# Performance work log

Measured on AMD Instinct MI355X. Metric: run time of the kernel, lower is better.

Reference implementation:

```python
import jax, jax.numpy as jnp
import numpy as np

B, N, P_EDGE = 2048, 64, 0.08


def setup_inputs() -> dict:
    key = jax.random.key(0)
    k1, _ = jax.random.split(key)
    u = jax.random.uniform(k1, (B, N, N))
    upper = jnp.triu(u < P_EDGE, k=1)
    A = (upper | jnp.swapaxes(upper, -1, -2)).astype(jnp.float32)  # symmetric, zero diag
    E = jnp.stack([1.0 - A, A], axis=-1)  # [B,N,N,2] one-hot edges
    node_mask = jnp.ones((B, N), dtype=jnp.float32)
    return {"E": E, "node_mask": node_mask}


def _diag(X):
    return jnp.diagonal(X, axis1=-2, axis2=-1)


def _trace(X):
    return _diag(X).sum(-1)


def reference(E, node_mask):
    A = E[..., 1:].sum(-1).astype(jnp.float32)  # [B,N,N]
    d = A.sum(-1)                               # degrees [B,N]
    k2 = A @ A
    k3 = k2 @ A
    k4 = k3 @ A
    k5 = k4 @ A
    k6 = k5 @ A

    c3 = _diag(k3)
    k3x = (c3 / 2)[..., None]
    k3y = (c3.sum(-1) / 6)[..., None]

    diag_a4 = _diag(k4)
    c4 = diag_a4 - d * (d - 1) - jnp.einsum('bij,bj->bi', A, d)
    k4x = (c4 / 2)[..., None]
    k4y = (c4.sum(-1) / 8)[..., None]

    diag_a5 = _diag(k5)
    tri = c3
    c5 = diag_a5 - 2 * tri * d - jnp.einsum('bij,bj->bi', A, tri) + tri
    k5x = (c5 / 2)[..., None]
    k5y = (c5.sum(-1) / 10)[..., None]

    t1 = _trace(k6)
    t2 = _trace(k3 ** 2)
    t3 = jnp.sum(A * k2 ** 2, axis=(-2, -1))
    d2 = _diag(k2)
    t4 = (d2 * diag_a4).sum(-1)
    t5 = _trace(k4)
    t6 = _trace(k3)
    t7 = (d2 ** 3).sum(-1)
    t8 = jnp.sum(k3, axis=(-2, -1))
    t9 = (d2 ** 2).sum(-1)
    t10 = _trace(k2)
    c6 = t1 - 3 * t2 + 9 * t3 - 6 * t4 + 6 * t5 - 4 * t6 + 4 * t7 + 3 * t8 - 12 * t9 + 4 * t10
    k6y = (c6 / 12)[..., None]

    x_cycles = jnp.concatenate([k3x, k4x, k5x], axis=-1)            # [B,N,3]
    y_cycles = jnp.concatenate([k3y, k4y, k5y, k6y], axis=-1)       # [B,4]

    x_cycles = x_cycles * node_mask[..., None] / 10.0
    y_cycles = y_cycles / 10.0
    x_cycles = jnp.minimum(x_cycles, 1.0)
    y_cycles = jnp.minimum(y_cycles, 1.0)
    return x_cycles, y_cycles
```

## Files before the change

### kernel.cpp

```cpp
#include <hip/hip_runtime.h>


typedef __attribute__((ext_vector_type(8))) short bf16x8;
typedef __attribute__((ext_vector_type(16))) float f32x16;

constexpr int BATCH = 2048;
constexpr int NN = 64;

__device__ __forceinline__ bf16x8 frag_ld(const unsigned short* buf, int row, int kb2) {
  const int idx = row * 64 + ((kb2 ^ (row & 7)) << 3);
  const uint4 v = *reinterpret_cast<const uint4*>(buf + idx);
  union { uint4 u; bf16x8 b; } cv; cv.u = v; return cv.b;
}

__global__ __launch_bounds__(64, 2) void node_cycle_kernel(
    const float4* __restrict__ E4,
    const float* __restrict__ nmask,
    float* __restrict__ out)
{
  const int b = blockIdx.x;
  const int lane = threadIdx.x;
  const int h = lane >> 5;
  const int c31 = lane & 31;

  __shared__ unsigned short bufA[64 * 64];
  __shared__ unsigned short bufK2[64 * 64];
  __shared__ float c3sh[NN];
  __shared__ uint2 rms[NN];

  const float4* __restrict__ Eb = E4 + (size_t)b * (NN * NN / 2);
  unsigned long long mA = 0ull, mB = 0ull;
  #pragma unroll
  for (int t = 0; t < 32; ++t) {
    const float4 f = Eb[t * 64 + lane];
    const int bit = 2 * t + h;
    mA |= (unsigned long long)(f.y > 0.5f) << bit;
    mB |= (unsigned long long)(f.w > 0.5f) << bit;
  }
  mA |= __shfl_xor(mA, 32);
  mB |= __shfl_xor(mB, 32);
  if (lane < 32) {
    rms[2 * lane]     = make_uint2((unsigned)mA, (unsigned)(mA >> 32));
    rms[2 * lane + 1] = make_uint2((unsigned)mB, (unsigned)(mB >> 32));
  }
  __syncthreads();
  const unsigned mlo = rms[lane].x, mhi = rms[lane].y;

  #pragma unroll
  for (int q = 0; q < 8; ++q) {
    unsigned w[4];
    #pragma unroll
    for (int p2 = 0; p2 < 4; ++p2) {
      const int c0 = q * 8 + p2 * 2;
      const unsigned b0 = (c0 < 32 ? (mlo >> c0) : (mhi >> (c0 - 32))) & 1u;
      const unsigned b1 = ((c0 + 1) < 32 ? (mlo >> (c0 + 1)) : (mhi >> (c0 + 1 - 32))) & 1u;
      w[p2] = (b0 ? 0x3F80u : 0u) | (b1 ? 0x3F800000u : 0u);
    }
    const int idx = lane * 64 + ((q ^ (lane & 7)) << 3);
    *reinterpret_cast<uint4*>(&bufA[idx]) = make_uint4(w[0], w[1], w[2], w[3]);
  }
  __syncthreads();

  bf16x8 Af[2][4];
  #pragma unroll
  for (int R = 0; R < 2; ++R)
    #pragma unroll
    for (int K = 0; K < 4; ++K)
      Af[R][K] = frag_ld(bufA, R * 32 + c31, 2 * K + h);

  f32x16 a00, a01, a10, a11;
  #pragma unroll
  for (int r = 0; r < 16; ++r) { a00[r] = 0.f; a01[r] = 0.f; a10[r] = 0.f; a11[r] = 0.f; }
  #pragma unroll
  for (int K = 0; K < 4; ++K) {
    a00 = __builtin_amdgcn_mfma_f32_32x32x16_bf16(Af[0][K], Af[0][K], a00, 0, 0, 0);
    a01 = __builtin_amdgcn_mfma_f32_32x32x16_bf16(Af[0][K], Af[1][K], a01, 0, 0, 0);
    a10 = __builtin_amdgcn_mfma_f32_32x32x16_bf16(Af[1][K], Af[0][K], a10, 0, 0, 0);
    a11 = __builtin_amdgcn_mfma_f32_32x32x16_bf16(Af[1][K], Af[1][K], a11, 0, 0, 0);
  }

  #define PACK_K2(ACC, R, C)                                                    \
  {                                                                             \
    const int c = (C) * 32 + c31;                                               \
    _Pragma("unroll")                                                           \
    for (int g = 0; g < 4; ++g) {                                               \
      const unsigned w0 = (__float_as_uint(ACC[4*g+1]) & 0xffff0000u) |         \
                          (__float_as_uint(ACC[4*g+0]) >> 16);                  \
      const unsigned w1 = (__float_as_uint(ACC[4*g+3]) & 0xffff0000u) |         \
                          (__float_as_uint(ACC[4*g+2]) >> 16);                  \
      const int bb = (4 * (R) + g) ^ (c & 7);                                   \
      *reinterpret_cast<uint2*>(&bufK2[c * 64 + bb * 8 + h * 4]) =              \
          make_uint2(w0, w1);                                                   \
    }                                                                           \
  }
  PACK_K2(a00, 0, 0) PACK_K2(a01, 0, 1) PACK_K2(a10, 1, 0) PACK_K2(a11, 1, 1)
  __syncthreads();

  bf16x8 Kf[2][4];
  #pragma unroll
  for (int R = 0; R < 2; ++R)
    #pragma unroll
    for (int K = 0; K < 4; ++K)
      Kf[R][K] = frag_ld(bufK2, R * 32 + c31, 2 * K + h);

  f32x16 d00, d01, d10, d11;
  #pragma unroll
  for (int r = 0; r < 16; ++r) { d00[r] = 0.f; d01[r] = 0.f; d10[r] = 0.f; d11[r] = 0.f; }
  #pragma unroll
  for (int K = 0; K < 4; ++K) {
    d00 = __builtin_amdgcn_mfma_f32_32x32x16_bf16(Kf[0][K], Af[0][K], d00, 0, 0, 0);
    d01 = __builtin_amdgcn_mfma_f32_32x32x16_bf16(Kf[0][K], Af[1][K], d01, 0, 0, 0);
    d10 = __builtin_amdgcn_mfma_f32_32x32x16_bf16(Kf[1][K], Af[0][K], d10, 0, 0, 0);
    d11 = __builtin_amdgcn_mfma_f32_32x32x16_bf16(Kf[1][K], Af[1][K], d11, 0, 0, 0);
  }

  float t1p = 0.f, t8p = 0.f;
  #define RED_T18(ACC)                                                          \
  { _Pragma("unroll") for (int r = 0; r < 16; ++r) {                            \
      const float v = ACC[r]; t1p = fmaf(v, v, t1p); t8p += v; } }
  RED_T18(d00) RED_T18(d01) RED_T18(d10) RED_T18(d11)

  const int dtarget = c31 - 4 * h;
  float c3d0 = 0.f, c3d1 = 0.f;
  #pragma unroll
  for (int r = 0; r < 16; ++r) {
    const int rowbase = (r & 3) + 8 * (r >> 2);
    c3d0 += (rowbase == dtarget) ? d00[r] : 0.f;
    c3d1 += (rowbase == dtarget) ? d11[r] : 0.f;
  }
  if (((c31 >> 2) & 1) == h) { c3sh[c31] = c3d0; c3sh[32 + c31] = c3d1; }

  #define PACK_K3(ACC, R, C)                                                    \
  {                                                                             \
    const int c = (C) * 32 + c31;                                               \
    _Pragma("unroll")                                                           \
    for (int g = 0; g < 4; ++g) {                                               \
      const unsigned u0 = ((unsigned)ACC[4*g+0]) | (((unsigned)ACC[4*g+1]) << 16); \
      const unsigned u1 = ((unsigned)ACC[4*g+2]) | (((unsigned)ACC[4*g+3]) << 16); \
      const int bb = (4 * (R) + g) ^ (c & 7);                                   \
      *reinterpret_cast<uint2*>(&bufA[c * 64 + bb * 8 + h * 4]) =               \
          make_uint2(u0, u1);                                                   \
    }                                                                           \
  }
  PACK_K3(d00, 0, 0) PACK_K3(d01, 0, 1) PACK_K3(d10, 1, 0) PACK_K3(d11, 1, 1)
  __syncthreads();

  float diag4 = 0.f, Ad = 0.f, diag5 = 0.f, t3p = 0.f, Atri = 0.f;
  #pragma unroll
  for (int bq = 0; bq < 8; ++bq) {
    const int idx = lane * 64 + ((bq ^ (lane & 7)) << 3);
    const uint4 vk2 = *reinterpret_cast<const uint4*>(&bufK2[idx]);
    const uint4 vk3 = *reinterpret_cast<const uint4*>(&bufA[idx]);
    const float4 c3a = *reinterpret_cast<const float4*>(&c3sh[bq * 8]);
    const float4 c3b = *reinterpret_cast<const float4*>(&c3sh[bq * 8 + 4]);
    const unsigned wk2[4] = {vk2.x, vk2.y, vk2.z, vk2.w};
    const unsigned wk3[4] = {vk3.x, vk3.y, vk3.z, vk3.w};
    const float c3v[8] = {c3a.x, c3a.y, c3a.z, c3a.w, c3b.x, c3b.y, c3b.z, c3b.w};
    #pragma unroll
    for (int e2 = 0; e2 < 4; ++e2) {
      const int j0 = bq * 8 + 2 * e2;
      const float k2lo = __uint_as_float(wk2[e2] << 16);
      const float k2hi = __uint_as_float(wk2[e2] & 0xffff0000u);
      const float k3lo = (float)(wk3[e2] & 0xffffu);
      const float k3hi = (float)(wk3[e2] >> 16);
      diag4 = fmaf(k2lo, k2lo, fmaf(k2hi, k2hi, diag4));
      Ad += k2lo + k2hi;
      diag5 = fmaf(k2lo, k3lo, fmaf(k2hi, k3hi, diag5));
      const unsigned b0 = (j0 < 32 ? (mlo >> j0) : (mhi >> (j0 - 32))) & 1u;
      const unsigned b1 = ((j0 + 1) < 32 ? (mlo >> (j0 + 1)) : (mhi >> (j0 + 1 - 32))) & 1u;
      const float s0 = b0 ? k2lo : 0.f;
      const float s1 = b1 ? k2hi : 0.f;
      t3p = fmaf(s0, k2lo, fmaf(s1, k2hi, t3p));
      Atri += (b0 ? c3v[2 * e2] : 0.f) + (b1 ? c3v[2 * e2 + 1] : 0.f);
    }
  }

  const float di  = (float)(__popc(mlo) + __popc(mhi));
  const float c3i = c3sh[lane];

  const float c4 = diag4 - di * (di - 1.f) - Ad;
  const float c5 = diag5 - 2.f * c3i * di - Atri + c3i;
  const float c6p = t1p + 3.f * t8p
            - 3.f * (c3i * c3i)
            + 9.f * t3p
            - 6.f * (di * diag4)
            + 6.f * diag4
            - 4.f * c3i
            + 4.f * (di * di * di)
            - 12.f * (di * di)
            + 4.f * di;

  float sc3 = c3i, sc4 = c4, sc5 = c5, sc6 = c6p;
  #pragma unroll
  for (int off = 32; off > 0; off >>= 1) {
    sc3 += __shfl_xor(sc3, off);
    sc4 += __shfl_xor(sc4, off);
    sc5 += __shfl_xor(sc5, off);
    sc6 += __shfl_xor(sc6, off);
  }

  const float m = nmask[b * NN + lane];
  float* xo = out + ((size_t)b * NN + lane) * 3;
  xo[0] = fminf(c3i * 0.5f * m * 0.1f, 1.f);
  xo[1] = fminf(c4 * 0.5f * m * 0.1f, 1.f);
  xo[2] = fminf(c5 * 0.5f * m * 0.1f, 1.f);

  if (lane == 0) {
    float4 y;
    y.x = fminf(sc3 * (1.f / 6.f)  * 0.1f, 1.f);
    y.y = fminf(sc4 * (1.f / 8.f)  * 0.1f, 1.f);
    y.z = fminf(sc5 * (1.f / 10.f) * 0.1f, 1.f);
    y.w = fminf(sc6 * (1.f / 12.f) * 0.1f, 1.f);
    *reinterpret_cast<float4*>(out + (size_t)BATCH * NN * 3 + b * 4) = y;
  }
}

extern "C" void kernel_launch(void* const* d_in, const int* in_sizes, int n_in,
                              void* d_out, int out_size, void* d_ws, size_t ws_size,
                              hipStream_t stream) {
  const float4* E4 = reinterpret_cast<const float4*>(d_in[0]);
  const float* nmask = reinterpret_cast<const float*>(d_in[1]);
  float* out = reinterpret_cast<float*>(d_out);
  node_cycle_kernel<<<BATCH, NN, 0, stream>>>(E4, nmask, out);
}
```

Baseline: 20.75 us.

## Split per-graph work across four wavefronts, one 32x32 MFMA tile each

Moves from one 64-thread wave per graph to four waves per block, each owning one 32x32 quadrant of the A^2 and A^3 products, with its own slice of the E load and bitmask build. The row reductions are split by column blocks across waves and combined through a shared accumulator array. The t1/t8 sums now come from the packed k3 values in the reduction pass rather than the MFMA accumulators. This raises memory-level parallelism and cuts per-wave serial MFMA chains, at the cost of extra block barriers and more LDS.

```diff
diff --git a/kernel.cpp b/kernel.cpp
--- a/kernel.cpp
+++ b/kernel.cpp
@@ -13,141 +13,139 @@
   union { uint4 u; bf16x8 b; } cv; cv.u = v; return cv.b;
 }
 
-__global__ __launch_bounds__(64, 2) void node_cycle_kernel(
+__global__ __launch_bounds__(256, 5) void node_cycle_kernel(
     const float4* __restrict__ E4,
     const float* __restrict__ nmask,
     float* __restrict__ out)
 {
   const int b = blockIdx.x;
-  const int lane = threadIdx.x;
+  const int tid = threadIdx.x;
+  const int lane = tid & 63;
+  const int w = tid >> 6;
   const int h = lane >> 5;
   const int c31 = lane & 31;
+  const int R = w >> 1, C = w & 1;
 
   __shared__ unsigned short bufA[64 * 64];
   __shared__ unsigned short bufK2[64 * 64];
+  __shared__ unsigned short sl[4][64];
+  __shared__ uint2 rms[NN];
   __shared__ float c3sh[NN];
-  __shared__ uint2 rms[NN];
+  __shared__ float accs[4][7][NN];
 
   const float4* __restrict__ Eb = E4 + (size_t)b * (NN * NN / 2);
-  unsigned long long mA = 0ull, mB = 0ull;
-  #pragma unroll
-  for (int t = 0; t < 32; ++t) {
-    const float4 f = Eb[t * 64 + lane];
-    const int bit = 2 * t + h;
-    mA |= (unsigned long long)(f.y > 0.5f) << bit;
-    mB |= (unsigned long long)(f.w > 0.5f) << bit;
-  }
-  mA |= __shfl_xor(mA, 32);
-  mB |= __shfl_xor(mB, 32);
+
+  unsigned mA = 0u, mB = 0u;
+  #pragma unroll
+  for (int q = 0; q < 8; ++q) {
+    const float4 f = Eb[w * 512 + q * 64 + lane];
+    const int bit = 2 * q + h;
+    mA |= (unsigned)(f.y > 0.5f) << bit;
+    mB |= (unsigned)(f.w > 0.5f) << bit;
+  }
+  mA |= (unsigned)__shfl_xor((int)mA, 32);
+  mB |= (unsigned)__shfl_xor((int)mB, 32);
   if (lane < 32) {
-    rms[2 * lane]     = make_uint2((unsigned)mA, (unsigned)(mA >> 32));
-    rms[2 * lane + 1] = make_uint2((unsigned)mB, (unsigned)(mB >> 32));
-  }
-  __syncthreads();
-  const unsigned mlo = rms[lane].x, mhi = rms[lane].y;
-
-  #pragma unroll
-  for (int q = 0; q < 8; ++q) {
-    unsigned w[4];
-    #pragma unroll
-    for (int p2 = 0; p2 < 4; ++p2) {
-      const int c0 = q * 8 + p2 * 2;
-      const unsigned b0 = (c0 < 32 ? (mlo >> c0) : (mhi >> (c0 - 32))) & 1u;
-      const unsigned b1 = ((c0 + 1) < 32 ? (mlo >> (c0 + 1)) : (mhi >> (c0 + 1 - 32))) & 1u;
-      w[p2] = (b0 ? 0x3F80u : 0u) | (b1 ? 0x3F800000u : 0u);
-    }
-    const int idx = lane * 64 + ((q ^ (lane & 7)) << 3);
-    *reinterpret_cast<uint4*>(&bufA[idx]) = make_uint4(w[0], w[1], w[2], w[3]);
-  }
-  __syncthreads();
-
-  bf16x8 Af[2][4];
-  #pragma unroll
-  for (int R = 0; R < 2; ++R)
-    #pragma unroll
-    for (int K = 0; K < 4; ++K)
-      Af[R][K] = frag_ld(bufA, R * 32 + c31, 2 * K + h);
-
-  f32x16 a00, a01, a10, a11;
-  #pragma unroll
-  for (int r = 0; r < 16; ++r) { a00[r] = 0.f; a01[r] = 0.f; a10[r] = 0.f; a11[r] = 0.f; }
+    sl[w][2 * lane]     = (unsigned short)mA;
+    sl[w][2 * lane + 1] = (unsigned short)mB;
+  }
+  __syncthreads();
+
+  if (tid < 128) {
+    const int c = tid >> 1, hf = tid & 1;
+    const unsigned v = (unsigned)sl[2 * hf][c] | ((unsigned)sl[2 * hf + 1][c] << 16);
+    if (hf == 0) rms[c].x = v; else rms[c].y = v;
+  }
+  __syncthreads();
+
+  const uint2 mr = rms[lane];
+
+  {
+    const unsigned word = (w < 2) ? mr.x : mr.y;
+    const unsigned bits16 = (word >> (16 * (w & 1))) & 0xffffu;
+    #pragma unroll
+    for (int e = 0; e < 2; ++e) {
+      const int bq = 2 * w + e;
+      unsigned wv[4];
+      #pragma unroll
+      for (int p2 = 0; p2 < 4; ++p2) {
+        const int c0 = e * 8 + p2 * 2;
+        const unsigned b0 = (bits16 >> c0) & 1u;
+        const unsigned b1 = (bits16 >> (c0 + 1)) & 1u;
+        wv[p2] = (b0 ? 0x3F80u : 0u) | (b1 ? 0x3F800000u : 0u);
+      }
+      const int idx = lane * 64 + ((bq ^ (lane & 7)) << 3);
+      *reinterpret_cast<uint4*>(&bufA[idx]) = make_uint4(wv[0], wv[1], wv[2], wv[3]);
+    }
+  }
+  __syncthreads();
+
+  bf16x8 Af[4], Bf[4];
   #pragma unroll
   for (int K = 0; K < 4; ++K) {
-    a00 = __builtin_amdgcn_mfma_f32_32x32x16_bf16(Af[0][K], Af[0][K], a00, 0, 0, 0);
-    a01 = __builtin_amdgcn_mfma_f32_32x32x16_bf16(Af[0][K], Af[1][K], a01, 0, 0, 0);
-    a10 = __builtin_amdgcn_mfma_f32_32x32x16_bf16(Af[1][K], Af[0][K], a10, 0, 0, 0);
-    a11 = __builtin_amdgcn_mfma_f32_32x32x16_bf16(Af[1][K], Af[1][K], a11, 0, 0, 0);
-  }
-
-  #define PACK_K2(ACC, R, C)                                                    \
-  {                                                                             \
-    const int c = (C) * 32 + c31;                                               \
-    _Pragma("unroll")                                                           \
-    for (int g = 0; g < 4; ++g) {                                               \
-      const unsigned w0 = (__float_as_uint(ACC[4*g+1]) & 0xffff0000u) |         \
-                          (__float_as_uint(ACC[4*g+0]) >> 16);                  \
-      const unsigned w1 = (__float_as_uint(ACC[4*g+3]) & 0xffff0000u) |         \
-                          (__float_as_uint(ACC[4*g+2]) >> 16);                  \
-      const int bb = (4 * (R) + g) ^ (c & 7);                                   \
-      *reinterpret_cast<uint2*>(&bufK2[c * 64 + bb * 8 + h * 4]) =              \
-          make_uint2(w0, w1);                                                   \
-    }                                                                           \
-  }
-  PACK_K2(a00, 0, 0) PACK_K2(a01, 0, 1) PACK_K2(a10, 1, 0) PACK_K2(a11, 1, 1)
-  __syncthreads();
-
-  bf16x8 Kf[2][4];
-  #pragma unroll
-  for (int R = 0; R < 2; ++R)
-    #pragma unroll
-    for (int K = 0; K < 4; ++K)
-      Kf[R][K] = frag_ld(bufK2, R * 32 + c31, 2 * K + h);
-
-  f32x16 d00, d01, d10, d11;
-  #pragma unroll
-  for (int r = 0; r < 16; ++r) { d00[r] = 0.f; d01[r] = 0.f; d10[r] = 0.f; d11[r] = 0.f; }
-  #pragma unroll
-  for (int K = 0; K < 4; ++K) {
-    d00 = __builtin_amdgcn_mfma_f32_32x32x16_bf16(Kf[0][K], Af[0][K], d00, 0, 0, 0);
-    d01 = __builtin_amdgcn_mfma_f32_32x32x16_bf16(Kf[0][K], Af[1][K], d01, 0, 0, 0);
-    d10 = __builtin_amdgcn_mfma_f32_32x32x16_bf16(Kf[1][K], Af[0][K], d10, 0, 0, 0);
-    d11 = __builtin_amdgcn_mfma_f32_32x32x16_bf16(Kf[1][K], Af[1][K], d11, 0, 0, 0);
-  }
-
+    Af[K] = frag_ld(bufA, R * 32 + c31, 2 * K + h);
+    Bf[K] = frag_ld(bufA, C * 32 + c31, 2 * K + h);
+  }
+  f32x16 acc;
+  #pragma unroll
+  for (int r = 0; r < 16; ++r) acc[r] = 0.f;
+  #pragma unroll
+  for (int K = 0; K < 4; ++K)
+    acc = __builtin_amdgcn_mfma_f32_32x32x16_bf16(Af[K], Bf[K], acc, 0, 0, 0);
+
+  {
+    const int c = C * 32 + c31;
+    #pragma unroll
+    for (int g = 0; g < 4; ++g) {
+      const unsigned w0 = (__float_as_uint(acc[4*g+1]) & 0xffff0000u) |
+                          (__float_as_uint(acc[4*g+0]) >> 16);
+      const unsigned w1 = (__float_as_uint(acc[4*g+3]) & 0xffff0000u) |
+                          (__float_as_uint(acc[4*g+2]) >> 16);
+      const int bb = (4 * R + g) ^ (c & 7);
+      *reinterpret_cast<uint2*>(&bufK2[c * 64 + bb * 8 + h * 4]) = make_uint2(w0, w1);
+    }
+  }
+  __syncthreads();
+
+  bf16x8 Kf[4];
+  #pragma unroll
+  for (int K = 0; K < 4; ++K)
+    Kf[K] = frag_ld(bufK2, R * 32 + c31, 2 * K + h);
+  f32x16 d;
+  #pragma unroll
+  for (int r = 0; r < 16; ++r) d[r] = 0.f;
+  #pragma unroll
+  for (int K = 0; K < 4; ++K)
+    d = __builtin_amdgcn_mfma_f32_32x32x16_bf16(Kf[K], Bf[K], d, 0, 0, 0);
+
+  if (R == C) {
+    const int dtarget = c31 - 4 * h;
+    float c3d = 0.f;
+    #pragma unroll
+    for (int r = 0; r < 16; ++r) {
+      const int rowbase = (r & 3) + 8 * (r >> 2);
+      c3d += (rowbase == dtarget) ? d[r] : 0.f;
+    }
+    if (((c31 >> 2) & 1) == h) c3sh[R * 32 + c31] = c3d;
+  }
+
+  {
+    const int c = C * 32 + c31;
+    #pragma unroll
+    for (int g = 0; g < 4; ++g) {
+      const unsigned u0 = ((unsigned)d[4*g+0]) | (((unsigned)d[4*g+1]) << 16);
+      const unsigned u1 = ((unsigned)d[4*g+2]) | (((unsigned)d[4*g+3]) << 16);
+      const int bb = (4 * R + g) ^ (c & 7);
+      *reinterpret_cast<uint2*>(&bufA[c * 64 + bb * 8 + h * 4]) = make_uint2(u0, u1);
+    }
+  }
+  __syncthreads();
+
+  float diag4 = 0.f, Ad = 0.f, diag5 = 0.f, t3p = 0.f, Atri = 0.f;
   float t1p = 0.f, t8p = 0.f;
-  #define RED_T18(ACC)                                                          \
-  { _Pragma("unroll") for (int r = 0; r < 16; ++r) {                            \
-      const float v = ACC[r]; t1p = fmaf(v, v, t1p); t8p += v; } }
-  RED_T18(d00) RED_T18(d01) RED_T18(d10) RED_T18(d11)
-
-  const int dtarget = c31 - 4 * h;
-  float c3d0 = 0.f, c3d1 = 0.f;
-  #pragma unroll
-  for (int r = 0; r < 16; ++r) {
-    const int rowbase = (r & 3) + 8 * (r >> 2);
-    c3d0 += (rowbase == dtarget) ? d00[r] : 0.f;
-    c3d1 += (rowbase == dtarget) ? d11[r] : 0.f;
-  }
-  if (((c31 >> 2) & 1) == h) { c3sh[c31] = c3d0; c3sh[32 + c31] = c3d1; }
-
-  #define PACK_K3(ACC, R, C)                                                    \
-  {                                                                             \
-    const int c = (C) * 32 + c31;                                               \
-    _Pragma("unroll")                                                           \
-    for (int g = 0; g < 4; ++g) {                                               \
-      const unsigned u0 = ((unsigned)ACC[4*g+0]) | (((unsigned)ACC[4*g+1]) << 16); \
-      const unsigned u1 = ((unsigned)ACC[4*g+2]) | (((unsigned)ACC[4*g+3]) << 16); \
-      const int bb = (4 * (R) + g) ^ (c & 7);                                   \
-      *reinterpret_cast<uint2*>(&bufA[c * 64 + bb * 8 + h * 4]) =               \
-          make_uint2(u0, u1);                                                   \
-    }                                                                           \
-  }
-  PACK_K3(d00, 0, 0) PACK_K3(d01, 0, 1) PACK_K3(d10, 1, 0) PACK_K3(d11, 1, 1)
-  __syncthreads();
-
-  float diag4 = 0.f, Ad = 0.f, diag5 = 0.f, t3p = 0.f, Atri = 0.f;
-  #pragma unroll
-  for (int bq = 0; bq < 8; ++bq) {
+  #pragma unroll
+  for (int e = 0; e < 2; ++e) {
+    const int bq = 2 * w + e;
     const int idx = lane * 64 + ((bq ^ (lane & 7)) << 3);
     const uint4 vk2 = *reinterpret_cast<const uint4*>(&bufK2[idx]);
     const uint4 vk3 = *reinterpret_cast<const uint4*>(&bufA[idx]);
@@ -166,52 +164,71 @@
       diag4 = fmaf(k2lo, k2lo, fmaf(k2hi, k2hi, diag4));
       Ad += k2lo + k2hi;
       diag5 = fmaf(k2lo, k3lo, fmaf(k2hi, k3hi, diag5));
-      const unsigned b0 = (j0 < 32 ? (mlo >> j0) : (mhi >> (j0 - 32))) & 1u;
-      const unsigned b1 = ((j0 + 1) < 32 ? (mlo >> (j0 + 1)) : (mhi >> (j0 + 1 - 32))) & 1u;
+      t1p = fmaf(k3lo, k3lo, fmaf(k3hi, k3hi, t1p));
+      t8p += k3lo + k3hi;
+      const unsigned b0 = (j0 < 32 ? (mr.x >> j0) : (mr.y >> (j0 - 32))) & 1u;
+      const unsigned b1 = ((j0 + 1) < 32 ? (mr.x >> (j0 + 1)) : (mr.y >> (j0 + 1 - 32))) & 1u;
       const float s0 = b0 ? k2lo : 0.f;
       const float s1 = b1 ? k2hi : 0.f;
       t3p = fmaf(s0, k2lo, fmaf(s1, k2hi, t3p));
       Atri += (b0 ? c3v[2 * e2] : 0.f) + (b1 ? c3v[2 * e2 + 1] : 0.f);
     }
   }
-
-  const float di  = (float)(__popc(mlo) + __popc(mhi));
-  const float c3i = c3sh[lane];
-
-  const float c4 = diag4 - di * (di - 1.f) - Ad;
-  const float c5 = diag5 - 2.f * c3i * di - Atri + c3i;
-  const float c6p = t1p + 3.f * t8p
-            - 3.f * (c3i * c3i)
-            + 9.f * t3p
-            - 6.f * (di * diag4)
-            + 6.f * diag4
-            - 4.f * c3i
-            + 4.f * (di * di * di)
-            - 12.f * (di * di)
-            + 4.f * di;
-
-  float sc3 = c3i, sc4 = c4, sc5 = c5, sc6 = c6p;
-  #pragma unroll
-  for (int off = 32; off > 0; off >>= 1) {
-    sc3 += __shfl_xor(sc3, off);
-    sc4 += __shfl_xor(sc4, off);
-    sc5 += __shfl_xor(sc5, off);
-    sc6 += __shfl_xor(sc6, off);
-  }
-
-  const float m = nmask[b * NN + lane];
-  float* xo = out + ((size_t)b * NN + lane) * 3;
-  xo[0] = fminf(c3i * 0.5f * m * 0.1f, 1.f);
-  xo[1] = fminf(c4 * 0.5f * m * 0.1f, 1.f);
-  xo[2] = fminf(c5 * 0.5f * m * 0.1f, 1.f);
-
-  if (lane == 0) {
-    float4 y;
-    y.x = fminf(sc3 * (1.f / 6.f)  * 0.1f, 1.f);
-    y.y = fminf(sc4 * (1.f / 8.f)  * 0.1f, 1.f);
-    y.z = fminf(sc5 * (1.f / 10.f) * 0.1f, 1.f);
-    y.w = fminf(sc6 * (1.f / 12.f) * 0.1f, 1.f);
-    *reinterpret_cast<float4*>(out + (size_t)BATCH * NN * 3 + b * 4) = y;
+  accs[w][0][lane] = diag4;
+  accs[w][1][lane] = Ad;
+  accs[w][2][lane] = diag5;
+  accs[w][3][lane] = t3p;
+  accs[w][4][lane] = Atri;
+  accs[w][5][lane] = t1p;
+  accs[w][6][lane] = t8p;
+  __syncthreads();
+
+  if (w == 0) {
+    float f[7];
+    #pragma unroll
+    for (int q2 = 0; q2 < 7; ++q2)
+      f[q2] = accs[0][q2][lane] + accs[1][q2][lane]
+            + accs[2][q2][lane] + accs[3][q2][lane];
+    const float diag4F = f[0], AdF = f[1], d5F = f[2], t3F = f[3],
+                AtF = f[4], t1F = f[5], t8F = f[6];
+    const float di  = (float)(__popc(mr.x) + __popc(mr.y));
+    const float c3i = c3sh[lane];
+
+    const float c4 = diag4F - di * (di - 1.f) - AdF;
+    const float c5 = d5F - 2.f * c3i * di - AtF + c3i;
+    const float c6p = t1F + 3.f * t8F
+              - 3.f * (c3i * c3i)
+              + 9.f * t3F
+              - 6.f * (di * diag4F)
+              + 6.f * diag4F
+              - 4.f * c3i
+              + 4.f * (di * di * di)
+              - 12.f * (di * di)
+              + 4.f * di;
+
+    float sc3 = c3i, sc4 = c4, sc5 = c5, sc6 = c6p;
+    #pragma unroll
+    for (int off = 32; off > 0; off >>= 1) {
+      sc3 += __shfl_xor(sc3, off);
+      sc4 += __shfl_xor(sc4, off);
+      sc5 += __shfl_xor(sc5, off);
+      sc6 += __shfl_xor(sc6, off);
+    }
+
+    const float m = nmask[b * NN + lane];
+    float* xo = out + ((size_t)b * NN + lane) * 3;
+    xo[0] = fminf(c3i * 0.5f * m * 0.1f, 1.f);
+    xo[1] = fminf(c4 * 0.5f * m * 0.1f, 1.f);
+    xo[2] = fminf(c5 * 0.5f * m * 0.1f, 1.f);
+
+    if (lane == 0) {
+      float4 y;
+      y.x = fminf(sc3 * (1.f / 6.f)  * 0.1f, 1.f);
+      y.y = fminf(sc4 * (1.f / 8.f)  * 0.1f, 1.f);
+      y.z = fminf(sc5 * (1.f / 10.f) * 0.1f, 1.f);
+      y.w = fminf(sc6 * (1.f / 12.f) * 0.1f, 1.f);
+      *reinterpret_cast<float4*>(out + (size_t)BATCH * NN * 3 + b * 4) = y;
+    }
   }
 }
 
@@ -221,5 +238,5 @@
   const float4* E4 = reinterpret_cast<const float4*>(d_in[0]);
   const float* nmask = reinterpret_cast<const float*>(d_in[1]);
   float* out = reinterpret_cast<float*>(d_out);
-  node_cycle_kernel<<<BATCH, NN, 0, stream>>>(E4, nmask, out);
+  node_cycle_kernel<<<BATCH, 256, 0, stream>>>(E4, nmask, out);
 }
```

New measurement: 19.30 us. -7.0%, faster.
